# Optimization experiments

Measured on AMD Instinct MI355X. Metric: run time of the kernel, lower is better.

The kernel has to match this reference:

```python
import jax, jax.numpy as jnp
import numpy as np

D, H, NL, DFF, VS, VT = 512, 8, 6, 2048, 32000, 32000
B, SS, ST = 4, 512, 512
PAD = 1
EPS = 1e-5


def _pos_encoding(S, d):
    pos = jnp.arange(S, dtype=jnp.float32)[:, None]
    div = jnp.exp(jnp.arange(0, d, 2, dtype=jnp.float32) * (-jnp.log(jnp.float32(10000.0)) / d))
    pe = jnp.zeros((S, d), dtype=jnp.float32)
    pe = pe.at[:, 0::2].set(jnp.sin(pos * div))
    pe = pe.at[:, 1::2].set(jnp.cos(pos * div))
    return pe


def _ln(x, g, b):
    m = jnp.mean(x, axis=-1, keepdims=True)
    v = jnp.mean(jnp.square(x - m), axis=-1, keepdims=True)
    return (x - m) * jax.lax.rsqrt(v + EPS) * g + b


def _mha(q, k, v, Wq, Wk, Wv, Wo, mask):
    # q,k,v: [B,S,D]; W*: [D,D] (torch Linear: y = x @ W.T); mask True -> masked
    Bq, Sq, _ = q.shape
    Sk = k.shape[1]
    dk = D // H
    Q = (q @ Wq.T).reshape(Bq, Sq, H, dk).transpose(0, 2, 1, 3)
    K = (k @ Wk.T).reshape(Bq, Sk, H, dk).transpose(0, 2, 1, 3)
    V = (v @ Wv.T).reshape(Bq, Sk, H, dk).transpose(0, 2, 1, 3)
    scores = jnp.einsum('bhqd,bhkd->bhqk', Q, K) / jnp.sqrt(jnp.float32(dk))
    scores = jnp.where(mask, -jnp.inf, scores)
    w = jax.nn.softmax(scores, axis=-1)
    w = jnp.nan_to_num(w)  # matches torch.nan_to_num after softmax of all -inf rows
    out = jnp.einsum('bhqk,bhkd->bhqd', w, V)
    out = out.transpose(0, 2, 1, 3).reshape(Bq, Sq, D)
    return out @ Wo.T


def _ffn(x, w1, b1, w2, b2):
    return jax.nn.relu(x @ w1.T + b1) @ w2.T + b2


def setup_inputs() -> dict:
    key = jax.random.key(0)
    ks = jax.random.split(key, 48)
    i = iter(range(48))
    n = lambda shape, s=0.02: jax.random.normal(ks[next(i)], shape, dtype=jnp.float32) * s
    inp = {
        'src': jax.random.randint(ks[next(i)], (B, SS), 0, VS),
        'tgt': jax.random.randint(ks[next(i)], (B, ST), 0, VT),
        'src_embed': n((VS, D)),
        'tgt_embed': n((VT, D)),
        'enc_Wq': n((NL, D, D)), 'enc_Wk': n((NL, D, D)), 'enc_Wv': n((NL, D, D)), 'enc_Wo': n((NL, D, D)),
        'enc_w1': n((NL, DFF, D)), 'enc_b1': jnp.zeros((NL, DFF)),
        'enc_w2': n((NL, D, DFF)), 'enc_b2': jnp.zeros((NL, D)),
        'enc_ln1g': jnp.ones((NL, D)), 'enc_ln1b': jnp.zeros((NL, D)),
        'enc_ln2g': jnp.ones((NL, D)), 'enc_ln2b': jnp.zeros((NL, D)),
        'enc_lnfg': jnp.ones((D,)), 'enc_lnfb': jnp.zeros((D,)),
        'dec_sWq': n((NL, D, D)), 'dec_sWk': n((NL, D, D)), 'dec_sWv': n((NL, D, D)), 'dec_sWo': n((NL, D, D)),
        'dec_cWq': n((NL, D, D)), 'dec_cWk': n((NL, D, D)), 'dec_cWv': n((NL, D, D)), 'dec_cWo': n((NL, D, D)),
        'dec_w1': n((NL, DFF, D)), 'dec_b1': jnp.zeros((NL, DFF)),
        'dec_w2': n((NL, D, DFF)), 'dec_b2': jnp.zeros((NL, D)),
        'dec_ln1g': jnp.ones((NL, D)), 'dec_ln1b': jnp.zeros((NL, D)),
        'dec_ln2g': jnp.ones((NL, D)), 'dec_ln2b': jnp.zeros((NL, D)),
        'dec_ln3g': jnp.ones((NL, D)), 'dec_ln3b': jnp.zeros((NL, D)),
        'dec_lnfg': jnp.ones((D,)), 'dec_lnfb': jnp.zeros((D,)),
        'out_W': n((VT, D)), 'out_b': jnp.zeros((VT,)),
    }
    return inp


def reference(src, tgt, src_embed, tgt_embed,
              enc_Wq, enc_Wk, enc_Wv, enc_Wo, enc_w1, enc_b1, enc_w2, enc_b2,
              enc_ln1g, enc_ln1b, enc_ln2g, enc_ln2b, enc_lnfg, enc_lnfb,
              dec_sWq, dec_sWk, dec_sWv, dec_sWo, dec_cWq, dec_cWk, dec_cWv, dec_cWo,
              dec_w1, dec_b1, dec_w2, dec_b2,
              dec_ln1g, dec_ln1b, dec_ln2g, dec_ln2b, dec_ln3g, dec_ln3b,
              dec_lnfg, dec_lnfb, out_W, out_b):
    scale = jnp.sqrt(jnp.float32(D))
    src_mask = (src == PAD)[:, None, None, :]                      # [B,1,1,SS]
    causal = jnp.triu(jnp.ones((ST, ST), dtype=bool), k=1)[None, None]
    tgt_mask = (tgt == PAD)[:, None, None, :] | causal             # [B,1,ST,ST]

    # Encoder
    x = src_embed[src] * scale + _pos_encoding(SS, D)[None]
    for l in range(NL):
        nrm = _ln(x, enc_ln1g[l], enc_ln1b[l])
        x = x + _mha(nrm, nrm, nrm, enc_Wq[l], enc_Wk[l], enc_Wv[l], enc_Wo[l], src_mask)
        x = x + _ffn(_ln(x, enc_ln2g[l], enc_ln2b[l]), enc_w1[l], enc_b1[l], enc_w2[l], enc_b2[l])
    memory = _ln(x, enc_lnfg, enc_lnfb)

    # Decoder
    y = tgt_embed[tgt] * scale + _pos_encoding(ST, D)[None]
    for l in range(NL):
        nrm = _ln(y, dec_ln1g[l], dec_ln1b[l])
        y = y + _mha(nrm, nrm, nrm, dec_sWq[l], dec_sWk[l], dec_sWv[l], dec_sWo[l], tgt_mask)
        nrm = _ln(y, dec_ln2g[l], dec_ln2b[l])
        y = y + _mha(nrm, memory, memory, dec_cWq[l], dec_cWk[l], dec_cWv[l], dec_cWo[l], src_mask)
        y = y + _ffn(_ln(y, dec_ln3g[l], dec_ln3b[l]), dec_w1[l], dec_b1[l], dec_w2[l], dec_b2[l])
    y = _ln(y, dec_lnfg, dec_lnfb)

    logits = y @ out_W.T + out_b                                   # [B,ST,VT]
    return logits
```

## Files before the change

### kernel.cpp

```cpp
#include <hip/hip_runtime.h>
#include <hip/hip_bf16.h>
#include <math.h>

#define Dm    512
#define Hh    8
#define NLay  6
#define DFFm  2048
#define Bb    4
#define NTOK  2048
#define PADID 1
#define LNEPS 1e-5f
#define S2W   262144

typedef __attribute__((ext_vector_type(8))) short short8;
typedef __attribute__((ext_vector_type(4))) float f32x4;
typedef unsigned short u16;

__device__ __forceinline__ u16 f2bf(float f) {
    union { float f; unsigned int i; } x; x.f = f;
    unsigned int r = x.i + 0x7fffu + ((x.i >> 16) & 1u);
    return (u16)(r >> 16);
}

typedef const __attribute__((address_space(1))) void* as1cv;
typedef __attribute__((address_space(3))) void* as3v;
__device__ __forceinline__ void gl_lds16(const u16* g, u16* l) {
    __builtin_amdgcn_global_load_lds((as1cv)g, (as3v)l, 16, 0, 0);
}

__device__ __forceinline__ void swz_tile(int& mt, int& nt) {
    const int nwg  = gridDim.x * gridDim.y;
    const int orig = blockIdx.y * gridDim.x + blockIdx.x;
    const int q8 = nwg >> 3, r8 = nwg & 7;
    const int xcd = orig & 7, idx = orig >> 3;
    const int wgid = (xcd < r8 ? xcd * (q8 + 1) : r8 * (q8 + 1) + (xcd - r8) * q8) + idx;
    const int MT = gridDim.y;
    mt = wgid % MT;
    nt = wgid / MT;
}

struct CvtJobs {
    const float* s[17];
    u16*         d[17];
    long         n4[17];
};
__global__ __launch_bounds__(256) void cvt_many(CvtJobs j) {
    const int job = blockIdx.y;
    const long n4 = j.n4[job];
    const float* in = j.s[job];
    u16* out = j.d[job];
    long i = (long)blockIdx.x * 256 + threadIdx.x;
    const long stride = (long)gridDim.x * 256;
    for (; i < n4; i += stride) {
        float4 v = ((const float4*)in)[i];
        ushort4 o;
        o.x = f2bf(v.x); o.y = f2bf(v.y); o.z = f2bf(v.z); o.w = f2bf(v.w);
        ((ushort4*)out)[i] = o;
    }
}

__global__ __launch_bounds__(256) void gemm_bt(
    const u16* __restrict__ A0, const u16* __restrict__ A1,
    const u16* __restrict__ A2, int lda,
    const u16* __restrict__ B0, const u16* __restrict__ B1,
    const u16* __restrict__ B2, int ldb,
    float* Cf, u16* Cb, int csm,
    const float* __restrict__ bias, int relu,
    int Kc, int ns, int vth, int koff, u16* vtp)
{
    __shared__ u16 As[2][4096];
    __shared__ u16 Bs[2][4096];
    int mt, nt; swz_tile(mt, nt);
    const int m0 = mt << 6, n0 = nt << 6;
    const int t = threadIdx.x, lane = t & 63, wave = t >> 6;
    const int wr = (wave >> 1) << 5, wc = (wave & 1) << 5;
    const int fr = lane & 15, fq = lane >> 4;
    const int srow = t >> 3;
    const int sch  = (t & 7) ^ (srow & 7);

    const int p = n0 >> 9;
    const u16* Amat = (p == 0) ? A0 : (p == 1 ? A1 : A2);
    const u16* Bmat; int nb;
    if (B1) { Bmat = (p == 0) ? B0 : (p == 1 ? B1 : B2); nb = n0 & 511; }
    else    { Bmat = B0; nb = n0; }
    const long kb = (long)blockIdx.z * Kc;

    const u16* Ag0 = Amat + (long)(m0 + srow) * lda + kb + (sch << 3);
    const u16* Ag1 = Ag0 + 32L * lda;
    const u16* Bg0 = Bmat + (long)(nb + srow) * ldb + kb + (sch << 3);
    const u16* Bg1 = Bg0 + 32L * ldb;

    f32x4 acc[2][2];
    #pragma unroll
    for (int i = 0; i < 2; i++)
        #pragma unroll
        for (int j = 0; j < 2; j++) acc[i][j] = (f32x4){0.f, 0.f, 0.f, 0.f};

    const int nk = Kc >> 6;
    gl_lds16(Ag0, &As[0][t << 3]);
    gl_lds16(Ag1, &As[0][(t + 256) << 3]);
    gl_lds16(Bg0, &Bs[0][t << 3]);
    gl_lds16(Bg1, &Bs[0][(t + 256) << 3]);
    __syncthreads();
    for (int ki = 0; ki < nk; ki++) {
        const int cur = ki & 1;
        if (ki + 1 < nk) {
            const int ko = (ki + 1) << 6;
            gl_lds16(Ag0 + ko, &As[cur ^ 1][t << 3]);
            gl_lds16(Ag1 + ko, &As[cur ^ 1][(t + 256) << 3]);
            gl_lds16(Bg0 + ko, &Bs[cur ^ 1][t << 3]);
            gl_lds16(Bg1 + ko, &Bs[cur ^ 1][(t + 256) << 3]);
        }
        const int r0 = wr + fr, r1 = wr + 16 + fr;
        const int c0 = wc + fr, c1 = wc + 16 + fr;
        #pragma unroll
        for (int h = 0; h < 2; h++) {
            const int lc = fq | (h << 2);
            short8 af0 = *(const short8*)&As[cur][(r0 << 6) + ((lc ^ (r0 & 7)) << 3)];
            short8 af1 = *(const short8*)&As[cur][(r1 << 6) + ((lc ^ (r1 & 7)) << 3)];
            short8 bf0 = *(const short8*)&Bs[cur][(c0 << 6) + ((lc ^ (c0 & 7)) << 3)];
            short8 bf1 = *(const short8*)&Bs[cur][(c1 << 6) + ((lc ^ (c1 & 7)) << 3)];
            acc[0][0] = __builtin_amdgcn_mfma_f32_16x16x32_bf16(af0, bf0, acc[0][0], 0, 0, 0);
            acc[0][1] = __builtin_amdgcn_mfma_f32_16x16x32_bf16(af0, bf1, acc[0][1], 0, 0, 0);
            acc[1][0] = __builtin_amdgcn_mfma_f32_16x16x32_bf16(af1, bf0, acc[1][0], 0, 0, 0);
            acc[1][1] = __builtin_amdgcn_mfma_f32_16x16x32_bf16(af1, bf1, acc[1][1], 0, 0, 0);
        }
        __syncthreads();
    }

    #pragma unroll
    for (int i = 0; i < 2; i++) {
        #pragma unroll
        for (int j = 0; j < 2; j++) {
            const int nl  = n0 + wc + (j << 4) + fr;
            const int mlb = m0 + wr + (i << 4) + (fq << 2);
            const float bsv = bias ? bias[nl] : 0.f;
            #pragma unroll
            for (int r = 0; r < 4; r++) {
                const int ml = mlb + r;
                if (ns > 1) {
                    float v = acc[i][j][r] + (blockIdx.z == 0 ? bsv : 0.f);
                    unsafeAtomicAdd(&Cf[(long)ml * csm + nl + koff], v);
                } else {
                    float v = acc[i][j][r] + bsv;
                    if (nl >= vth) {
                        vtp[(long)(ml >> 9) * S2W + (long)(nl - vth) * 512 + (ml & 511)] = f2bf(v);
                    } else {
                        if (relu) v = fmaxf(v, 0.f);
                        long ci = (long)ml * csm + nl + koff;
                        if (Cf) Cf[ci] = v;
                        if (Cb) Cb[ci] = f2bf(v);
                    }
                }
            }
        }
    }
}

__global__ __launch_bounds__(256) void gemm_big(
    const u16* __restrict__ A, int lda,
    const u16* __restrict__ B, int ldb,
    float* Cf, u16* Cb, int ldc,
    const float* __restrict__ bias, int relu, int K)
{
    __shared__ u16 As[2][4096];
    __shared__ u16 Bs[2][4096];
    int mt, nt; swz_tile(mt, nt);
    const int m0 = mt << 7, n0 = nt << 7;
    const int t = threadIdx.x, lane = t & 63, wave = t >> 6;
    const int wr = (wave >> 1) << 6, wc = (wave & 1) << 6;
    const int fr = lane & 15, fq = lane >> 4;
    const int srow = t >> 2;
    const int sch  = (t & 3) ^ ((srow >> 1) & 3);
    const u16* Ag0 = A + (long)(m0 + srow) * lda + (sch << 3);
    const u16* Ag1 = A + (long)(m0 + 64 + srow) * lda + (sch << 3);
    const u16* Bg0 = B + (long)(n0 + srow) * ldb + (sch << 3);
    const u16* Bg1 = B + (long)(n0 + 64 + srow) * ldb + (sch << 3);

    f32x4 acc[4][4];
    #pragma unroll
    for (int i = 0; i < 4; i++)
        #pragma unroll
        for (int j = 0; j < 4; j++) acc[i][j] = (f32x4){0.f, 0.f, 0.f, 0.f};

    const int nk = K >> 5;
    gl_lds16(Ag0, &As[0][t << 3]);
    gl_lds16(Ag1, &As[0][(t + 256) << 3]);
    gl_lds16(Bg0, &Bs[0][t << 3]);
    gl_lds16(Bg1, &Bs[0][(t + 256) << 3]);
    __syncthreads();
    for (int ki = 0; ki < nk; ki++) {
        const int cur = ki & 1;
        if (ki + 1 < nk) {
            const int ko = (ki + 1) << 5;
            gl_lds16(Ag0 + ko, &As[cur ^ 1][t << 3]);
            gl_lds16(Ag1 + ko, &As[cur ^ 1][(t + 256) << 3]);
            gl_lds16(Bg0 + ko, &Bs[cur ^ 1][t << 3]);
            gl_lds16(Bg1 + ko, &Bs[cur ^ 1][(t + 256) << 3]);
        }
        short8 af[4], bf[4];
        #pragma unroll
        for (int i = 0; i < 4; i++) {
            const int r = wr + (i << 4) + fr;
            af[i] = *(const short8*)&As[cur][(r << 5) + ((fq ^ ((r >> 1) & 3)) << 3)];
        }
        #pragma unroll
        for (int j = 0; j < 4; j++) {
            const int c = wc + (j << 4) + fr;
            bf[j] = *(const short8*)&Bs[cur][(c << 5) + ((fq ^ ((c >> 1) & 3)) << 3)];
        }
        #pragma unroll
        for (int i = 0; i < 4; i++)
            #pragma unroll
            for (int j = 0; j < 4; j++)
                acc[i][j] = __builtin_amdgcn_mfma_f32_16x16x32_bf16(af[i], bf[j], acc[i][j], 0, 0, 0);
        __syncthreads();
    }

    #pragma unroll
    for (int i = 0; i < 4; i++) {
        #pragma unroll
        for (int j = 0; j < 4; j++) {
            const int nl  = n0 + wc + (j << 4) + fr;
            const int mlb = m0 + wr + (i << 4) + (fq << 2);
            const float bsv = bias ? bias[nl] : 0.f;
            #pragma unroll
            for (int r = 0; r < 4; r++) {
                float v = acc[i][j][r] + bsv;
                if (relu) v = fmaxf(v, 0.f);
                long ci = (long)(mlb + r) * ldc + nl;
                if (Cf) Cf[ci] = v;
                if (Cb) Cb[ci] = f2bf(v);
            }
        }
    }
}

__global__ __launch_bounds__(256) void attn_fused(
    const u16* __restrict__ qkb, const u16* __restrict__ vt,
    const int* __restrict__ ids, u16* __restrict__ attc, int causal)
{
    __shared__ u16 Ks[2][4096];
    __shared__ u16 Vs[2][4096];
    __shared__ short Ps[4][16][72];
    const int t = threadIdx.x, lane = t & 63, w = t >> 6;
    const int fr = lane & 15, fq = lane >> 4;
    const int q0 = blockIdx.x << 6, h = blockIdx.y, b = blockIdx.z;

    const u16* qp = qkb + (long)(b * 512 + q0 + (w << 4) + fr) * 1024 + h * 64 + (fq << 3);
    short8 aq0 = *(const short8*)qp;
    short8 aq1 = *(const short8*)(qp + 32);

    const int sr = t >> 3, sc = (t & 7) ^ (sr & 7);
    const u16* kg0 = qkb + (long)(b * 512 + sr) * 1024 + 512 + h * 64 + (sc << 3);
    const u16* kg1 = kg0 + 32L * 1024;
    const u16* vg0 = vt + (long)b * S2W + (long)(h * 64 + sr) * 512 + (sc << 3);
    const u16* vg1 = vg0 + 32L * 512;

    unsigned pmask = 0;
    #pragma unroll
    for (int kt = 0; kt < 8; kt++)
        #pragma unroll
        for (int j = 0; j < 4; j++)
            if (ids[b * 512 + (kt << 6) + (j << 4) + fr] == PADID)
                pmask |= 1u << ((kt << 2) + j);

    float m[4], l[4]; f32x4 oc[4];
    #pragma unroll
    for (int r = 0; r < 4; r++) { m[r] = -INFINITY; l[r] = 0.f; oc[r] = (f32x4){0.f,0.f,0.f,0.f}; }

    const int lastkt = causal ? (q0 >> 6) : 7;
    auto stage = [&](int kt, int buf) {
        const long so = (long)(kt << 6);
        gl_lds16(kg0 + so * 1024, &Ks[buf][t << 3]);
        gl_lds16(kg1 + so * 1024, &Ks[buf][(t + 256) << 3]);
        gl_lds16(vg0 + so, &Vs[buf][t << 3]);
        gl_lds16(vg1 + so, &Vs[buf][(t + 256) << 3]);
    };
    stage(0, 0);
    __syncthreads();

    for (int kt = 0; kt <= lastkt; kt++) {
        const int cur = kt & 1;
        if (kt < lastkt) stage(kt + 1, cur ^ 1);

        f32x4 sc4[4];
        #pragma unroll
        for (int j = 0; j < 4; j++) sc4[j] = (f32x4){0.f,0.f,0.f,0.f};
        #pragma unroll
        for (int j = 0; j < 4; j++) {
            const int rr = (j << 4) + fr;
            short8 bk0 = *(const short8*)&Ks[cur][rr * 64 + ((fq ^ (rr & 7)) << 3)];
            short8 bk1 = *(const short8*)&Ks[cur][rr * 64 + (((fq | 4) ^ (rr & 7)) << 3)];
            sc4[j] = __builtin_amdgcn_mfma_f32_16x16x32_bf16(aq0, bk0, sc4[j], 0, 0, 0);
            sc4[j] = __builtin_amdgcn_mfma_f32_16x16x32_bf16(aq1, bk1, sc4[j], 0, 0, 0);
        }
        const int s0 = kt << 6;
        #pragma unroll
        for (int r = 0; r < 4; r++) {
            const int qa = q0 + (w << 4) + (fq << 2) + r;
            float mx = -INFINITY;
            #pragma unroll
            for (int j = 0; j < 4; j++) {
                bool msk = ((pmask >> ((kt << 2) + j)) & 1) ||
                           (causal && (s0 + (j << 4) + fr) > qa);
                float sv = msk ? -INFINITY : sc4[j][r] * 0.125f;
                sc4[j][r] = sv;
                mx = fmaxf(mx, sv);
            }
            mx = fmaxf(mx, __shfl_xor(mx, 1)); mx = fmaxf(mx, __shfl_xor(mx, 2));
            mx = fmaxf(mx, __shfl_xor(mx, 4)); mx = fmaxf(mx, __shfl_xor(mx, 8));
            float mnew  = fmaxf(m[r], mx);
            float scale = (mnew == -INFINITY) ? 1.f : __expf(m[r] - mnew);
            float ps = 0.f;
            #pragma unroll
            for (int j = 0; j < 4; j++) {
                float p = (sc4[j][r] == -INFINITY) ? 0.f : __expf(sc4[j][r] - mnew);
                sc4[j][r] = p; ps += p;
            }
            ps += __shfl_xor(ps, 1); ps += __shfl_xor(ps, 2);
            ps += __shfl_xor(ps, 4); ps += __shfl_xor(ps, 8);
            l[r] = l[r] * scale + ps;
            m[r] = mnew;
            #pragma unroll
            for (int j2 = 0; j2 < 4; j2++) oc[j2][r] *= scale;
        }
        #pragma unroll
        for (int r = 0; r < 4; r++)
            #pragma unroll
            for (int j = 0; j < 4; j++)
                Ps[w][(fq << 2) + r][(j << 4) + fr] = (short)f2bf(sc4[j][r]);
        #pragma unroll
        for (int kc = 0; kc < 2; kc++) {
            short8 pa = *(const short8*)&Ps[w][fr][(kc << 5) + (fq << 3)];
            #pragma unroll
            for (int j2 = 0; j2 < 4; j2++) {
                const int rd = (j2 << 4) + fr;
                const int cch = (((kc << 2) | fq) ^ (rd & 7));
                short8 bv = *(const short8*)&Vs[cur][rd * 64 + (cch << 3)];
                oc[j2] = __builtin_amdgcn_mfma_f32_16x16x32_bf16(pa, bv, oc[j2], 0, 0, 0);
            }
        }
        __syncthreads();
    }

    float inv[4];
    #pragma unroll
    for (int r = 0; r < 4; r++) inv[r] = (l[r] > 0.f) ? 1.f / l[r] : 0.f;
    #pragma unroll
    for (int j2 = 0; j2 < 4; j2++)
        #pragma unroll
        for (int r = 0; r < 4; r++)
            attc[(long)(b * 512 + q0 + (w << 4) + (fq << 2) + r) * 512 + h * 64 + (j2 << 4) + fr]
                = f2bf(oc[j2][r] * inv[r]);
}

__global__ __launch_bounds__(256) void ln_rows(
    const float* __restrict__ x, const float* __restrict__ g,
    const float* __restrict__ b, u16* __restrict__ out)
{
    int row  = blockIdx.x * 4 + (threadIdx.x >> 6);
    int lane = threadIdx.x & 63;
    const float* xr = x + (long)row * Dm;
    float v[8]; float s = 0.f;
    #pragma unroll
    for (int i = 0; i < 8; i++) { v[i] = xr[lane + (i << 6)]; s += v[i]; }
    #pragma unroll
    for (int o = 32; o > 0; o >>= 1) s += __shfl_xor(s, o);
    float mean = s * (1.f / 512.f);
    float q = 0.f;
    #pragma unroll
    for (int i = 0; i < 8; i++) { float d = v[i] - mean; q += d * d; }
    #pragma unroll
    for (int o = 32; o > 0; o >>= 1) q += __shfl_xor(q, o);
    float rinv = rsqrtf(q * (1.f / 512.f) + LNEPS);
    u16* orow = out + (long)row * Dm;
    #pragma unroll
    for (int i = 0; i < 8; i++) {
        int c = lane + (i << 6);
        orow[c] = f2bf((v[i] - mean) * rinv * g[c] + b[c]);
    }
}

__global__ __launch_bounds__(256) void embed_pe(
    const int* __restrict__ ids, const float* __restrict__ emb,
    float* __restrict__ out)
{
    int idx = blockIdx.x * 256 + threadIdx.x;
    int d   = idx & 511;
    int tok = idx >> 9;
    int s   = tok & 511;
    int id  = ids[tok];
    float val = emb[(long)id * Dm + d] * 22.62741699796952f;
    int i2 = d >> 1;
    float dv  = expf((float)(i2 << 1) * (-9.210340371976184f / 512.f));
    float ang = (float)s * dv;
    val += (d & 1) ? cosf(ang) : sinf(ang);
    out[idx] = val;
}

extern "C" void kernel_launch(void* const* d_in, const int* in_sizes, int n_in,
                              void* d_out, int out_size, void* d_ws, size_t ws_size,
                              hipStream_t stream)
{
    (void)in_sizes; (void)n_in; (void)out_size; (void)ws_size;
    const int*   src       = (const int*)d_in[0];
    const int*   tgt       = (const int*)d_in[1];
    const float* src_embed = (const float*)d_in[2];
    const float* tgt_embed = (const float*)d_in[3];
    const float* enc_b1  = (const float*)d_in[9];
    const float* enc_b2  = (const float*)d_in[11];
    const float* enc_ln1g = (const float*)d_in[12];
    const float* enc_ln1b = (const float*)d_in[13];
    const float* enc_ln2g = (const float*)d_in[14];
    const float* enc_ln2b = (const float*)d_in[15];
    const float* enc_lnfg = (const float*)d_in[16];
    const float* enc_lnfb = (const float*)d_in[17];
    const float* dec_b1  = (const float*)d_in[27];
    const float* dec_b2  = (const float*)d_in[29];
    const float* dec_ln1g = (const float*)d_in[30];
    const float* dec_ln1b = (const float*)d_in[31];
    const float* dec_ln2g = (const float*)d_in[32];
    const float* dec_ln2b = (const float*)d_in[33];
    const float* dec_ln3g = (const float*)d_in[34];
    const float* dec_ln3b = (const float*)d_in[35];
    const float* dec_lnfg = (const float*)d_in[36];
    const float* dec_lnfb = (const float*)d_in[37];
    const float* out_b  = (const float*)d_in[39];

    char* wp = (char*)d_ws;
    auto carve = [&](size_t nbytes) {
        void* p = (void*)wp; wp += (nbytes + 255) & ~(size_t)255; return p;
    };

    const long nW = (long)NLay * S2W;
    const long nF = (long)NLay * DFFm * Dm;
    const long nO = 32000L * Dm;

    u16* Wb[12];
    for (int i = 0; i < 12; i++) Wb[i] = (u16*)carve((size_t)nW * 2);
    u16* w1E  = (u16*)carve((size_t)nF * 2);
    u16* w2E  = (u16*)carve((size_t)nF * 2);
    u16* w1D  = (u16*)carve((size_t)nF * 2);
    u16* w2D  = (u16*)carve((size_t)nF * 2);
    u16* outW = (u16*)carve((size_t)nO * 2);

    float* x  = (float*)carve((size_t)NTOK * Dm * 4);
    float* y  = (float*)carve((size_t)NTOK * Dm * 4);
    u16* nrm  = (u16*)carve((size_t)NTOK * Dm * 2);
    u16* qkb  = (u16*)carve((size_t)NTOK * 1024 * 2);
    u16* vt   = (u16*)carve((size_t)Bb * Dm * 512 * 2);
    u16* attc = (u16*)carve((size_t)NTOK * Dm * 2);
    u16* h1   = (u16*)carve((size_t)NTOK * DFFm * 2);
    u16* memn = (u16*)carve((size_t)NTOK * Dm * 2);

    const int wi[12] = {4, 5, 6, 7, 18, 19, 20, 21, 22, 23, 24, 25};
    CvtJobs jobs;
    for (int i = 0; i < 12; i++) {
        jobs.s[i] = (const float*)d_in[wi[i]]; jobs.d[i] = Wb[i]; jobs.n4[i] = nW >> 2;
    }
    jobs.s[12] = (const float*)d_in[8];  jobs.d[12] = w1E;  jobs.n4[12] = nF >> 2;
    jobs.s[13] = (const float*)d_in[10]; jobs.d[13] = w2E;  jobs.n4[13] = nF >> 2;
    jobs.s[14] = (const float*)d_in[26]; jobs.d[14] = w1D;  jobs.n4[14] = nF >> 2;
    jobs.s[15] = (const float*)d_in[28]; jobs.d[15] = w2D;  jobs.n4[15] = nF >> 2;
    jobs.s[16] = (const float*)d_in[38]; jobs.d[16] = outW; jobs.n4[16] = nO >> 2;
    cvt_many<<<dim3(512, 17), 256, 0, stream>>>(jobs);

    const int BIG = 1 << 28;
    u16 *eWq = Wb[0], *eWk = Wb[1], *eWv = Wb[2], *eWo = Wb[3];
    u16 *sWq = Wb[4], *sWk = Wb[5], *sWv = Wb[6], *sWo = Wb[7];
    u16 *cWq = Wb[8], *cWk = Wb[9], *cWv = Wb[10], *cWo = Wb[11];

    embed_pe<<<4096, 256, 0, stream>>>(src, src_embed, x);
    for (int l = 0; l < NLay; l++) {
        const size_t wo = (size_t)l * S2W;
        ln_rows<<<512, 256, 0, stream>>>(x, enc_ln1g + l * Dm, enc_ln1b + l * Dm, nrm);
        gemm_bt<<<dim3(24, 32, 1), 256, 0, stream>>>(nrm, nrm, nrm, 512,
            eWq + wo, eWk + wo, eWv + wo, 512,
            nullptr, qkb, 1024, nullptr, 0, 512, 1, 1024, 0, vt);
        attn_fused<<<dim3(8, Hh, Bb), 256, 0, stream>>>(qkb, vt, src, attc, 0);
        gemm_bt<<<dim3(8, 32, 2), 256, 0, stream>>>(attc, attc, attc, 512,
            eWo + wo, nullptr, nullptr, 512,
            x, nullptr, 512, nullptr, 0, 256, 2, BIG, 0, nullptr);
        ln_rows<<<512, 256, 0, stream>>>(x, enc_ln2g + l * Dm, enc_ln2b + l * Dm, nrm);
        gemm_bt<<<dim3(32, 32, 1), 256, 0, stream>>>(nrm, nrm, nrm, 512,
            w1E + (size_t)l * DFFm * Dm, nullptr, nullptr, 512,
            nullptr, h1, DFFm, enc_b1 + l * DFFm, 1, 512, 1, BIG, 0, nullptr);
        gemm_bt<<<dim3(8, 32, 4), 256, 0, stream>>>(h1, h1, h1, DFFm,
            w2E + (size_t)l * Dm * DFFm, nullptr, nullptr, DFFm,
            x, nullptr, 512, enc_b2 + l * Dm, 0, 512, 4, BIG, 0, nullptr);
    }
    ln_rows<<<512, 256, 0, stream>>>(x, enc_lnfg, enc_lnfb, memn);

    embed_pe<<<4096, 256, 0, stream>>>(tgt, tgt_embed, y);
    for (int l = 0; l < NLay; l++) {
        const size_t wo = (size_t)l * S2W;
        ln_rows<<<512, 256, 0, stream>>>(y, dec_ln1g + l * Dm, dec_ln1b + l * Dm, nrm);
        gemm_bt<<<dim3(24, 32, 1), 256, 0, stream>>>(nrm, nrm, nrm, 512,
            sWq + wo, sWk + wo, sWv + wo, 512,
            nullptr, qkb, 1024, nullptr, 0, 512, 1, 1024, 0, vt);
        attn_fused<<<dim3(8, Hh, Bb), 256, 0, stream>>>(qkb, vt, tgt, attc, 1);
        gemm_bt<<<dim3(8, 32, 2), 256, 0, stream>>>(attc, attc, attc, 512,
            sWo + wo, nullptr, nullptr, 512,
            y, nullptr, 512, nullptr, 0, 256, 2, BIG, 0, nullptr);
        ln_rows<<<512, 256, 0, stream>>>(y, dec_ln2g + l * Dm, dec_ln2b + l * Dm, nrm);
        gemm_bt<<<dim3(24, 32, 1), 256, 0, stream>>>(nrm, memn, memn, 512,
            cWq + wo, cWk + wo, cWv + wo, 512,
            nullptr, qkb, 1024, nullptr, 0, 512, 1, 1024, 0, vt);
        attn_fused<<<dim3(8, Hh, Bb), 256, 0, stream>>>(qkb, vt, src, attc, 0);
        gemm_bt<<<dim3(8, 32, 2), 256, 0, stream>>>(attc, attc, attc, 512,
            cWo + wo, nullptr, nullptr, 512,
            y, nullptr, 512, nullptr, 0, 256, 2, BIG, 0, nullptr);
        ln_rows<<<512, 256, 0, stream>>>(y, dec_ln3g + l * Dm, dec_ln3b + l * Dm, nrm);
        gemm_bt<<<dim3(32, 32, 1), 256, 0, stream>>>(nrm, nrm, nrm, 512,
            w1D + (size_t)l * DFFm * Dm, nullptr, nullptr, 512,
            nullptr, h1, DFFm, dec_b1 + l * DFFm, 1, 512, 1, BIG, 0, nullptr);
        gemm_bt<<<dim3(8, 32, 4), 256, 0, stream>>>(h1, h1, h1, DFFm,
            w2D + (size_t)l * Dm * DFFm, nullptr, nullptr, DFFm,
            y, nullptr, 512, dec_b2 + l * Dm, 0, 512, 4, BIG, 0, nullptr);
    }
    ln_rows<<<512, 256, 0, stream>>>(y, dec_lnfg, dec_lnfb, nrm);

    gemm_big<<<dim3(250, 16), 256, 0, stream>>>(nrm, 512, outW, 512,
        (float*)d_out, nullptr, 32000, out_b, 0, 512);
}
```

Measured before the change: 1.648 ms.

## Batch cross-attention K/V projections for all layers; triple-buffer vocab GEMM

Adds a gemm_kv6 kernel that computes the cross-attention K and V projections of the encoder memory for all six decoder layers in one launch. Each decoder layer then only projects Q, and attn_fused takes a separate K pointer and stride. The output-vocab GEMM moves to a three-stage LDS pipeline with vmcnt-based waits, and the Wo split-K factor rises from 2 to 4. The goal is fewer small launches and better load/compute overlap, at the cost of extra scratch memory and more atomic adds.

```diff
diff --git a/kernel.cpp b/kernel.cpp
--- a/kernel.cpp
+++ b/kernel.cpp
@@ -27,6 +27,12 @@
 __device__ __forceinline__ void gl_lds16(const u16* g, u16* l) {
     __builtin_amdgcn_global_load_lds((as1cv)g, (as3v)l, 16, 0, 0);
 }
+
+#define SYNC_VM(N) do { \
+    asm volatile("s_waitcnt vmcnt(" #N ")" ::: "memory"); \
+    __builtin_amdgcn_s_barrier(); \
+    __builtin_amdgcn_sched_barrier(0); \
+} while (0)
 
 __device__ __forceinline__ void swz_tile(int& mt, int& nt) {
     const int nwg  = gridDim.x * gridDim.y;
@@ -157,14 +163,96 @@
     }
 }
 
+__global__ __launch_bounds__(256) void gemm_kv6(
+    const u16* __restrict__ A,
+    const u16* __restrict__ Wk, const u16* __restrict__ Wv,
+    u16* __restrict__ kc, u16* __restrict__ vtc)
+{
+    __shared__ u16 As[2][4096];
+    __shared__ u16 Bs[2][4096];
+    int mt, nt; swz_tile(mt, nt);
+    const int m0 = mt << 6, n0 = nt << 6;
+    const int z = blockIdx.z;
+    const int t = threadIdx.x, lane = t & 63, wave = t >> 6;
+    const int wr = (wave >> 1) << 5, wc = (wave & 1) << 5;
+    const int fr = lane & 15, fq = lane >> 4;
+    const int srow = t >> 3;
+    const int sch  = (t & 7) ^ (srow & 7);
+
+    const int p = n0 >> 9;
+    const u16* Bmat = ((p == 0) ? Wk : Wv) + (size_t)z * S2W;
+    const int nb = n0 & 511;
+
+    const u16* Ag0 = A + (long)(m0 + srow) * 512 + (sch << 3);
+    const u16* Ag1 = Ag0 + 32L * 512;
+    const u16* Bg0 = Bmat + (long)(nb + srow) * 512 + (sch << 3);
+    const u16* Bg1 = Bg0 + 32L * 512;
+
+    f32x4 acc[2][2];
+    #pragma unroll
+    for (int i = 0; i < 2; i++)
+        #pragma unroll
+        for (int j = 0; j < 2; j++) acc[i][j] = (f32x4){0.f, 0.f, 0.f, 0.f};
+
+    gl_lds16(Ag0, &As[0][t << 3]);
+    gl_lds16(Ag1, &As[0][(t + 256) << 3]);
+    gl_lds16(Bg0, &Bs[0][t << 3]);
+    gl_lds16(Bg1, &Bs[0][(t + 256) << 3]);
+    __syncthreads();
+    for (int ki = 0; ki < 8; ki++) {
+        const int cur = ki & 1;
+        if (ki + 1 < 8) {
+            const int ko = (ki + 1) << 6;
+            gl_lds16(Ag0 + ko, &As[cur ^ 1][t << 3]);
+            gl_lds16(Ag1 + ko, &As[cur ^ 1][(t + 256) << 3]);
+            gl_lds16(Bg0 + ko, &Bs[cur ^ 1][t << 3]);
+            gl_lds16(Bg1 + ko, &Bs[cur ^ 1][(t + 256) << 3]);
+        }
+        const int r0 = wr + fr, r1 = wr + 16 + fr;
+        const int c0 = wc + fr, c1 = wc + 16 + fr;
+        #pragma unroll
+        for (int h = 0; h < 2; h++) {
+            const int lc = fq | (h << 2);
+            short8 af0 = *(const short8*)&As[cur][(r0 << 6) + ((lc ^ (r0 & 7)) << 3)];
+            short8 af1 = *(const short8*)&As[cur][(r1 << 6) + ((lc ^ (r1 & 7)) << 3)];
+            short8 bf0 = *(const short8*)&Bs[cur][(c0 << 6) + ((lc ^ (c0 & 7)) << 3)];
+            short8 bf1 = *(const short8*)&Bs[cur][(c1 << 6) + ((lc ^ (c1 & 7)) << 3)];
+            acc[0][0] = __builtin_amdgcn_mfma_f32_16x16x32_bf16(af0, bf0, acc[0][0], 0, 0, 0);
+            acc[0][1] = __builtin_amdgcn_mfma_f32_16x16x32_bf16(af0, bf1, acc[0][1], 0, 0, 0);
+            acc[1][0] = __builtin_amdgcn_mfma_f32_16x16x32_bf16(af1, bf0, acc[1][0], 0, 0, 0);
+            acc[1][1] = __builtin_amdgcn_mfma_f32_16x16x32_bf16(af1, bf1, acc[1][1], 0, 0, 0);
+        }
+        __syncthreads();
+    }
+
+    #pragma unroll
+    for (int i = 0; i < 2; i++) {
+        #pragma unroll
+        for (int j = 0; j < 2; j++) {
+            const int nl  = n0 + wc + (j << 4) + fr;
+            const int mlb = m0 + wr + (i << 4) + (fq << 2);
+            #pragma unroll
+            for (int r = 0; r < 4; r++) {
+                const int ml = mlb + r;
+                const u16 v = f2bf(acc[i][j][r]);
+                if (nl < 512)
+                    kc[(long)z * NTOK * 512 + (long)ml * 512 + nl] = v;
+                else
+                    vtc[(long)z * Bb * S2W + (long)(ml >> 9) * S2W +
+                        (long)(nl - 512) * 512 + (ml & 511)] = v;
+            }
+        }
+    }
+}
+
 __global__ __launch_bounds__(256) void gemm_big(
     const u16* __restrict__ A, int lda,
     const u16* __restrict__ B, int ldb,
-    float* Cf, u16* Cb, int ldc,
-    const float* __restrict__ bias, int relu, int K)
+    float* Cf, int ldc,
+    const float* __restrict__ bias, int K)
 {
-    __shared__ u16 As[2][4096];
-    __shared__ u16 Bs[2][4096];
+    __shared__ u16 As[3][4096];
+    __shared__ u16 Bs[3][4096];
     int mt, nt; swz_tile(mt, nt);
     const int m0 = mt << 7, n0 = nt << 7;
     const int t = threadIdx.x, lane = t & 63, wave = t >> 6;
@@ -184,20 +272,21 @@
         for (int j = 0; j < 4; j++) acc[i][j] = (f32x4){0.f, 0.f, 0.f, 0.f};
 
     const int nk = K >> 5;
-    gl_lds16(Ag0, &As[0][t << 3]);
-    gl_lds16(Ag1, &As[0][(t + 256) << 3]);
-    gl_lds16(Bg0, &Bs[0][t << 3]);
-    gl_lds16(Bg1, &Bs[0][(t + 256) << 3]);
-    __syncthreads();
+    auto stage = [&](int ki, int buf) {
+        const int ko = ki << 5;
+        gl_lds16(Ag0 + ko, &As[buf][t << 3]);
+        gl_lds16(Ag1 + ko, &As[buf][(t + 256) << 3]);
+        gl_lds16(Bg0 + ko, &Bs[buf][t << 3]);
+        gl_lds16(Bg1 + ko, &Bs[buf][(t + 256) << 3]);
+    };
+    stage(0, 0);
+    if (nk > 1) { stage(1, 1); SYNC_VM(4); }
+    else        { SYNC_VM(0); }
+
+    int cur = 0;
     for (int ki = 0; ki < nk; ki++) {
-        const int cur = ki & 1;
-        if (ki + 1 < nk) {
-            const int ko = (ki + 1) << 5;
-            gl_lds16(Ag0 + ko, &As[cur ^ 1][t << 3]);
-            gl_lds16(Ag1 + ko, &As[cur ^ 1][(t + 256) << 3]);
-            gl_lds16(Bg0 + ko, &Bs[cur ^ 1][t << 3]);
-            gl_lds16(Bg1 + ko, &Bs[cur ^ 1][(t + 256) << 3]);
-        }
+        const bool st = (ki + 2 < nk);
+        if (st) stage(ki + 2, cur == 0 ? 2 : cur - 1);
         short8 af[4], bf[4];
         #pragma unroll
         for (int i = 0; i < 4; i++) {
@@ -214,7 +303,11 @@
             #pragma unroll
             for (int j = 0; j < 4; j++)
                 acc[i][j] = __builtin_amdgcn_mfma_f32_16x16x32_bf16(af[i], bf[j], acc[i][j], 0, 0, 0);
-        __syncthreads();
+        if (ki + 1 < nk) {
+            if (st) SYNC_VM(4);
+            else    SYNC_VM(0);
+        }
+        cur = (cur == 2) ? 0 : cur + 1;
     }
 
     #pragma unroll
@@ -225,19 +318,15 @@
             const int mlb = m0 + wr + (i << 4) + (fq << 2);
             const float bsv = bias ? bias[nl] : 0.f;
             #pragma unroll
-            for (int r = 0; r < 4; r++) {
-                float v = acc[i][j][r] + bsv;
-                if (relu) v = fmaxf(v, 0.f);
-                long ci = (long)(mlb + r) * ldc + nl;
-                if (Cf) Cf[ci] = v;
-                if (Cb) Cb[ci] = f2bf(v);
-            }
+            for (int r = 0; r < 4; r++)
+                Cf[(long)(mlb + r) * ldc + nl] = acc[i][j][r] + bsv;
         }
     }
 }
 
 __global__ __launch_bounds__(256) void attn_fused(
-    const u16* __restrict__ qkb, const u16* __restrict__ vt,
+    const u16* __restrict__ qkb, const u16* __restrict__ kb_, int ldk,
+    const u16* __restrict__ vt,
     const int* __restrict__ ids, u16* __restrict__ attc, int causal)
 {
     __shared__ u16 Ks[2][4096];
@@ -252,8 +341,8 @@
     short8 aq1 = *(const short8*)(qp + 32);
 
     const int sr = t >> 3, sc = (t & 7) ^ (sr & 7);
-    const u16* kg0 = qkb + (long)(b * 512 + sr) * 1024 + 512 + h * 64 + (sc << 3);
-    const u16* kg1 = kg0 + 32L * 1024;
+    const u16* kg0 = kb_ + (long)(b * 512 + sr) * ldk + h * 64 + (sc << 3);
+    const u16* kg1 = kg0 + 32L * ldk;
     const u16* vg0 = vt + (long)b * S2W + (long)(h * 64 + sr) * 512 + (sc << 3);
     const u16* vg1 = vg0 + 32L * 512;
 
@@ -272,8 +361,8 @@
     const int lastkt = causal ? (q0 >> 6) : 7;
     auto stage = [&](int kt, int buf) {
         const long so = (long)(kt << 6);
-        gl_lds16(kg0 + so * 1024, &Ks[buf][t << 3]);
-        gl_lds16(kg1 + so * 1024, &Ks[buf][(t + 256) << 3]);
+        gl_lds16(kg0 + so * ldk, &Ks[buf][t << 3]);
+        gl_lds16(kg1 + so * ldk, &Ks[buf][(t + 256) << 3]);
         gl_lds16(vg0 + so, &Vs[buf][t << 3]);
         gl_lds16(vg1 + so, &Vs[buf][(t + 256) << 3]);
     };
@@ -315,8 +404,8 @@
             float ps = 0.f;
             #pragma unroll
             for (int j = 0; j < 4; j++) {
-                float p = (sc4[j][r] == -INFINITY) ? 0.f : __expf(sc4[j][r] - mnew);
-                sc4[j][r] = p; ps += p;
+                float p2 = (sc4[j][r] == -INFINITY) ? 0.f : __expf(sc4[j][r] - mnew);
+                sc4[j][r] = p2; ps += p2;
             }
             ps += __shfl_xor(ps, 1); ps += __shfl_xor(ps, 2);
             ps += __shfl_xor(ps, 4); ps += __shfl_xor(ps, 8);
@@ -331,12 +420,12 @@
             for (int j = 0; j < 4; j++)
                 Ps[w][(fq << 2) + r][(j << 4) + fr] = (short)f2bf(sc4[j][r]);
         #pragma unroll
-        for (int kc = 0; kc < 2; kc++) {
-            short8 pa = *(const short8*)&Ps[w][fr][(kc << 5) + (fq << 3)];
+        for (int kc2 = 0; kc2 < 2; kc2++) {
+            short8 pa = *(const short8*)&Ps[w][fr][(kc2 << 5) + (fq << 3)];
             #pragma unroll
             for (int j2 = 0; j2 < 4; j2++) {
                 const int rd = (j2 << 4) + fr;
-                const int cch = (((kc << 2) | fq) ^ (rd & 7));
+                const int cch = (((kc2 << 2) | fq) ^ (rd & 7));
                 short8 bv = *(const short8*)&Vs[cur][rd * 64 + (cch << 3)];
                 oc[j2] = __builtin_amdgcn_mfma_f32_16x16x32_bf16(pa, bv, oc[j2], 0, 0, 0);
             }
@@ -453,6 +542,8 @@
     u16* attc = (u16*)carve((size_t)NTOK * Dm * 2);
     u16* h1   = (u16*)carve((size_t)NTOK * DFFm * 2);
     u16* memn = (u16*)carve((size_t)NTOK * Dm * 2);
+    u16* kc6  = (u16*)carve((size_t)NLay * NTOK * 512 * 2);
+    u16* vt6  = (u16*)carve((size_t)NLay * Bb * S2W * 2);
 
     const int wi[12] = {4, 5, 6, 7, 18, 19, 20, 21, 22, 23, 24, 25};
     CvtJobs jobs;
@@ -478,10 +569,10 @@
         gemm_bt<<<dim3(24, 32, 1), 256, 0, stream>>>(nrm, nrm, nrm, 512,
             eWq + wo, eWk + wo, eWv + wo, 512,
             nullptr, qkb, 1024, nullptr, 0, 512, 1, 1024, 0, vt);
-        attn_fused<<<dim3(8, Hh, Bb), 256, 0, stream>>>(qkb, vt, src, attc, 0);
-        gemm_bt<<<dim3(8, 32, 2), 256, 0, stream>>>(attc, attc, attc, 512,
+        attn_fused<<<dim3(8, Hh, Bb), 256, 0, stream>>>(qkb, qkb + 512, 1024, vt, src, attc, 0);
+        gemm_bt<<<dim3(8, 32, 4), 256, 0, stream>>>(attc, attc, attc, 512,
             eWo + wo, nullptr, nullptr, 512,
-            x, nullptr, 512, nullptr, 0, 256, 2, BIG, 0, nullptr);
+            x, nullptr, 512, nullptr, 0, 128, 4, BIG, 0, nullptr);
         ln_rows<<<512, 256, 0, stream>>>(x, enc_ln2g + l * Dm, enc_ln2b + l * Dm, nrm);
         gemm_bt<<<dim3(32, 32, 1), 256, 0, stream>>>(nrm, nrm, nrm, 512,
             w1E + (size_t)l * DFFm * Dm, nullptr, nullptr, 512,
@@ -491,6 +582,7 @@
             x, nullptr, 512, enc_b2 + l * Dm, 0, 512, 4, BIG, 0, nullptr);
     }
     ln_rows<<<512, 256, 0, stream>>>(x, enc_lnfg, enc_lnfb, memn);
+    gemm_kv6<<<dim3(16, 32, NLay), 256, 0, stream>>>(memn, cWk, cWv, kc6, vt6);
 
     embed_pe<<<4096, 256, 0, stream>>>(tgt, tgt_embed, y);
     for (int l = 0; l < NLay; l++) {
@@ -499,18 +591,19 @@
         gemm_bt<<<dim3(24, 32, 1), 256, 0, stream>>>(nrm, nrm, nrm, 512,
             sWq + wo, sWk + wo, sWv + wo, 512,
             nullptr, qkb, 1024, nullptr, 0, 512, 1, 1024, 0, vt);
-        attn_fused<<<dim3(8, Hh, Bb), 256, 0, stream>>>(qkb, vt, tgt, attc, 1);
-        gemm_bt<<<dim3(8, 32, 2), 256, 0, stream>>>(attc, attc, attc, 512,
+        attn_fused<<<dim3(8, Hh, Bb), 256, 0, stream>>>(qkb, qkb + 512, 1024, vt, tgt, attc, 1);
+        gemm_bt<<<dim3(8, 32, 4), 256, 0, stream>>>(attc, attc, attc, 512,
             sWo + wo, nullptr, nullptr, 512,
-            y, nullptr, 512, nullptr, 0, 256, 2, BIG, 0, nullptr);
+            y, nullptr, 512, nullptr, 0, 128, 4, BIG, 0, nullptr);
         ln_rows<<<512, 256, 0, stream>>>(y, dec_ln2g + l * Dm, dec_ln2b + l * Dm, nrm);
-        gemm_bt<<<dim3(24, 32, 1), 256, 0, stream>>>(nrm, memn, memn, 512,
-            cWq + wo, cWk + wo, cWv + wo, 512,
-            nullptr, qkb, 1024, nullptr, 0, 512, 1, 1024, 0, vt);
-        attn_fused<<<dim3(8, Hh, Bb), 256, 0, stream>>>(qkb, vt, src, attc, 0);
-        gemm_bt<<<dim3(8, 32, 2), 256, 0, stream>>>(attc, attc, attc, 512,
+        gemm_bt<<<dim3(8, 32, 1), 256, 0, stream>>>(nrm, nrm, nrm, 512,
+            cWq + wo, nullptr, nullptr, 512,
+            nullptr, qkb, 1024, nullptr, 0, 512, 1, BIG, 0, nullptr);
+        attn_fused<<<dim3(8, Hh, Bb), 256, 0, stream>>>(qkb,
+            kc6 + (size_t)l * NTOK * 512, 512, vt6 + (size_t)l * Bb * S2W, src, attc, 0);
+        gemm_bt<<<dim3(8, 32, 4), 256, 0, stream>>>(attc, attc, attc, 512,
             cWo + wo, nullptr, nullptr, 512,
-            y, nullptr, 512, nullptr, 0, 256, 2, BIG, 0, nullptr);
+            y, nullptr, 512, nullptr, 0, 128, 4, BIG, 0, nullptr);
         ln_rows<<<512, 256, 0, stream>>>(y, dec_ln3g + l * Dm, dec_ln3b + l * Dm, nrm);
         gemm_bt<<<dim3(32, 32, 1), 256, 0, stream>>>(nrm, nrm, nrm, 512,
             w1D + (size_t)l * DFFm * Dm, nullptr, nullptr, 512,
@@ -522,5 +615,5 @@
     ln_rows<<<512, 256, 0, stream>>>(y, dec_lnfg, dec_lnfb, nrm);
 
     gemm_big<<<dim3(250, 16), 256, 0, stream>>>(nrm, 512, outW, 512,
-        (float*)d_out, nullptr, 32000, out_b, 0, 512);
-}
+        (float*)d_out, 32000, out_b, 512);
+}
```

After: 1.753 ms. 1.06x slower.
